# Kernel optimization log

Hardware: AMD Instinct MI355X
Metric: run time of the kernel (lower is better)

The kernel has to match this reference:

```python
import jax, jax.numpy as jnp
import numpy as np

B, N, VF, EF, DV, DE, LN = 64, 64, 32, 16, 128, 128, 4
EPS_INNER = 128.0  # BatchNorm1d(MAX_N, internal_d_vert): 2nd positional arg is eps (faithful to source bug)
EPS_BN = 1e-5


def gev_layer(v_in, e_in, evW, evb, eW, eb, vW, vb, relu=True):
    act = jax.nn.relu if relu else (lambda x: x)
    ev = v_in @ evW + evb                                   # [B,N,De]
    # outer_v_sum: ev.unsqueeze(1) + ev.unsqueeze(2) -> [B,N,N,De]
    e_out = act(e_in @ eW + eb + ev[:, None, :, :] + ev[:, :, None, :])
    per_v_e = e_out.sum(axis=1)                             # sum-aggregate over dim 1
    v_out = act(jnp.concatenate([per_v_e, v_in], axis=-1) @ vW + vb)
    return v_out, e_out


def bn_flat(v, g, b):
    # BatchNorm1d(N*VF) on [B, N*VF] in training mode (biased var)
    x = v.reshape(-1, N * VF)
    mu = x.mean(axis=0)
    var = x.var(axis=0)
    x = (x - mu) * jax.lax.rsqrt(var + EPS_BN) * g + b
    return x.reshape(-1, N, VF)


def bn_inner(v, g, b):
    # BatchNorm1d(MAX_N, eps=128) on [B, N, D]: channels are the N axis, stats over (B, D)
    mu = v.mean(axis=(0, 2), keepdims=True)
    var = v.var(axis=(0, 2), keepdims=True)
    return (v - mu) * jax.lax.rsqrt(var + EPS_INNER) * g[None, :, None] + b[None, :, None]


def setup_inputs() -> dict:
    key = jax.random.key(0)
    ks = jax.random.split(key, 24)
    s = 0.01  # force_lin_init with init_noise=0.01, biases zero
    nrm = lambda k, shp: jax.random.normal(k, shp, dtype=jnp.float32) * s
    inp = {
        "v": jax.random.normal(ks[0], (B, N, VF), dtype=jnp.float32),
        "e": jax.random.normal(ks[1], (B, N, N, EF), dtype=jnp.float32),
        "bn_in_g": jnp.ones((N * VF,), jnp.float32),
        "bn_in_b": jnp.zeros((N * VF,), jnp.float32),
        "g1_evW": nrm(ks[2], (VF, DE)), "g1_evb": jnp.zeros((DE,), jnp.float32),
        "g1_eW": nrm(ks[3], (EF, DE)), "g1_eb": jnp.zeros((DE,), jnp.float32),
        "g1_vW": nrm(ks[4], (VF + DE, DV)), "g1_vb": jnp.zeros((DV,), jnp.float32),
        "inn_evW": nrm(ks[5], (LN, DV, DE)), "inn_evb": jnp.zeros((LN, DE), jnp.float32),
        "inn_eW": nrm(ks[6], (LN, DE, DE)), "inn_eb": jnp.zeros((LN, DE), jnp.float32),
        "inn_vW": nrm(ks[7], (LN, DV + DE, DV)), "inn_vb": jnp.zeros((LN, DV), jnp.float32),
        "bn_g": jnp.ones((LN, N), jnp.float32),
        "bn_b": jnp.zeros((LN, N), jnp.float32),
        "g3_evW": nrm(ks[8], (DV, 1)), "g3_evb": jnp.zeros((1,), jnp.float32),
        "g3_eW": nrm(ks[9], (DE, 1)), "g3_eb": jnp.zeros((1,), jnp.float32),
        "g3_vW": nrm(ks[10], (DV + 1, 1)), "g3_vb": jnp.zeros((1,), jnp.float32),
    }
    return inp


def reference(v, e, bn_in_g, bn_in_b, g1_evW, g1_evb, g1_eW, g1_eb, g1_vW, g1_vb,
              inn_evW, inn_evb, inn_eW, inn_eb, inn_vW, inn_vb, bn_g, bn_b,
              g3_evW, g3_evb, g3_eW, g3_eb, g3_vW, g3_vb):
    v = bn_flat(v, bn_in_g, bn_in_b)
    v, e = gev_layer(v, e, g1_evW, g1_evb, g1_eW, g1_eb, g1_vW, g1_vb)
    for i in range(LN):
        v_next, e_next = gev_layer(v, e, inn_evW[i], inn_evb[i], inn_eW[i], inn_eb[i], inn_vW[i], inn_vb[i])
        v = v_next + v  # resnet
        e = e_next + e
        v = bn_inner(v, bn_g[i], bn_b[i])
    v, e = gev_layer(v, e, g3_evW, g3_evb, g3_eW, g3_eb, g3_vW, g3_vb, relu=False)
    return v, e
```

## Files before the change

### kernel.cpp

```cpp
#include <hip/hip_runtime.h>
#include <hip/hip_bf16.h>


typedef __bf16 bf16_t;
typedef __bf16 bf16x8 __attribute__((ext_vector_type(8)));
typedef __bf16 bf16x4 __attribute__((ext_vector_type(4)));
typedef float f32x4 __attribute__((ext_vector_type(4)));

__device__ __forceinline__ void bar_lgkm() {
  asm volatile("s_waitcnt lgkmcnt(0)\n\ts_barrier" ::: "memory");
}

__global__ __launch_bounds__(256) void k_prep(const float* __restrict__ vin,
    const float* __restrict__ g, const float* __restrict__ bt,
    const float* __restrict__ eW, float* __restrict__ v0,
    bf16_t* __restrict__ Wt, float* __restrict__ stats) {
  const int blk = blockIdx.x, tid = threadIdx.x;
  if (blk < 8) {
    int ch = blk * 256 + tid;
    float s = 0.f, s2 = 0.f;
    for (int b = 0; b < 64; ++b) { float x = vin[b * 2048 + ch]; s += x; s2 += x * x; }
    float mu = s * (1.f / 64.f);
    float var = s2 * (1.f / 64.f) - mu * mu;
    float sc = rsqrtf(var + 1e-5f) * g[ch];
    float bb = bt[ch];
    for (int b = 0; b < 64; ++b) {
      float x = vin[b * 2048 + ch];
      v0[b * 2048 + ch] = (x - mu) * sc + bb;
    }
  } else if (blk < 264) {
    int idx = (blk - 8) * 256 + tid;
    int l = idx >> 14, r = idx & 16383, n = r >> 7, k = r & 127;
    Wt[idx] = (bf16_t)eW[(l << 14) + (k << 7) + n];
  } else {
    for (int i = tid; i < 512; i += 256) stats[i] = 0.f;
  }
}

template <int K>
__global__ __launch_bounds__(256) void k_ev(const float* __restrict__ v_in,
    const float* __restrict__ W, const float* __restrict__ bias,
    float* __restrict__ out) {
  __shared__ float rows_s[8][K];
  const int r0 = blockIdx.x * 8;
  const int tid = threadIdx.x;
  const int c = tid & 127, h = tid >> 7;
  for (int idx = tid; idx < 8 * K; idx += 256) {
    int rr = idx / K, kk = idx % K;
    rows_s[rr][kk] = v_in[(r0 + rr) * K + kk];
  }
  __syncthreads();
  float acc[4];
  const float bv = bias[c];
#pragma unroll
  for (int r = 0; r < 4; ++r) acc[r] = bv;
  for (int k4 = 0; k4 < K; k4 += 4) {
    float w0 = W[(k4 + 0) * 128 + c], w1 = W[(k4 + 1) * 128 + c];
    float w2 = W[(k4 + 2) * 128 + c], w3 = W[(k4 + 3) * 128 + c];
#pragma unroll
    for (int r = 0; r < 4; ++r) {
      float4 x = *(const float4*)&rows_s[h * 4 + r][k4];
      acc[r] += x.x * w0 + x.y * w1 + x.z * w2 + x.w * w3;
    }
  }
#pragma unroll
  for (int r = 0; r < 4; ++r) out[(r0 + h * 4 + r) * 128 + c] = acc[r];
}

__global__ __launch_bounds__(256) void k_evbn(float* __restrict__ v,
    const float* __restrict__ stats, const float* __restrict__ g,
    const float* __restrict__ bt, const float* __restrict__ W,
    const float* __restrict__ bias, float* __restrict__ out) {
  __shared__ float rows_s[8][128];
  const int r0 = blockIdx.x * 8;
  const int tid = threadIdx.x;
  const int c = tid & 127, h = tid >> 7;
#pragma unroll
  for (int u = 0; u < 4; ++u) {
    int idx = u * 256 + tid;
    int rr = idx >> 7, k = idx & 127;
    int n = (r0 + rr) & 63;
    float mu = stats[n] * (1.f / 8192.f);
    float var = stats[64 + n] * (1.f / 8192.f) - mu * mu;
    float sc = rsqrtf(var + 128.f) * g[n];
    float x = (v[(r0 + rr) * 128 + k] - mu) * sc + bt[n];
    rows_s[rr][k] = x;
    v[(r0 + rr) * 128 + k] = x;
  }
  __syncthreads();
  float acc[4];
  const float bv = bias[c];
#pragma unroll
  for (int r = 0; r < 4; ++r) acc[r] = bv;
  for (int k4 = 0; k4 < 128; k4 += 4) {
    float w0 = W[(k4 + 0) * 128 + c], w1 = W[(k4 + 1) * 128 + c];
    float w2 = W[(k4 + 2) * 128 + c], w3 = W[(k4 + 3) * 128 + c];
#pragma unroll
    for (int r = 0; r < 4; ++r) {
      float4 x = *(const float4*)&rows_s[h * 4 + r][k4];
      acc[r] += x.x * w0 + x.y * w1 + x.z * w2 + x.w * w3;
    }
  }
#pragma unroll
  for (int r = 0; r < 4; ++r) out[(r0 + h * 4 + r) * 128 + c] = acc[r];
}

__global__ __launch_bounds__(256) void k_edge_g1(const float* __restrict__ e0,
    const float* __restrict__ eW, const float* __restrict__ eb,
    const float* __restrict__ ev, bf16_t* __restrict__ e_ws,
    float* __restrict__ pve) {
  __shared__ bf16_t A0s[2][64][40];
  __shared__ bf16_t Os[2][64][136];
  const int b = blockIdx.x >> 5, j0 = (blockIdx.x & 31) * 2;
  const int tid = threadIdx.x;
  const int lane = tid & 63, w = tid >> 6;
  const int quad = lane >> 4, l16 = lane & 15;
#pragma unroll
  for (int t = 0; t < 2; ++t) {
    int idx = tid + t * 256;
    int row = idx >> 3, off = (idx & 7) * 4;
    int jc = off >> 4, k = off & 15;
    f32x4 x = *(const f32x4*)&e0[((b * 64 + row) * 64 + j0) * 16 + off];
    bf16x4 y;
#pragma unroll
    for (int r = 0; r < 4; ++r) y[r] = (bf16_t)x[r];
    *(bf16x4*)&A0s[jc][row][k] = y;
    bf16x4 z = {(bf16_t)0.f, (bf16_t)0.f, (bf16_t)0.f, (bf16_t)0.f};
    *(bf16x4*)&A0s[jc][row][16 + k] = z;
  }
  const int c0[2] = {w * 32 + quad * 4, w * 32 + 16 + quad * 4};
  bf16x8 wf[2];
#pragma unroll
  for (int nt = 0; nt < 2; ++nt) {
    const int c = w * 32 + nt * 16 + l16;
#pragma unroll
    for (int jj = 0; jj < 8; ++jj)
      wf[nt][jj] = (quad < 2) ? (bf16_t)eW[(quad * 8 + jj) * 128 + c] : (bf16_t)0.f;
  }
  f32x4 acc[2][4][2];
  {
    f32x4 ebv[2], evj[2][2], evi[4][2];
#pragma unroll
    for (int nt = 0; nt < 2; ++nt) {
      ebv[nt] = *(const f32x4*)&eb[c0[nt]];
#pragma unroll
      for (int jc = 0; jc < 2; ++jc)
        evj[jc][nt] = *(const f32x4*)&ev[(b * 64 + j0 + jc) * 128 + c0[nt]];
#pragma unroll
      for (int mt = 0; mt < 4; ++mt)
        evi[mt][nt] = *(const f32x4*)&ev[(b * 64 + mt * 16 + l16) * 128 + c0[nt]];
    }
#pragma unroll
    for (int jc = 0; jc < 2; ++jc)
#pragma unroll
      for (int mt = 0; mt < 4; ++mt)
#pragma unroll
        for (int nt = 0; nt < 2; ++nt)
          acc[jc][mt][nt] = ebv[nt] + evj[jc][nt] + evi[mt][nt];
  }
  __syncthreads();
#pragma unroll
  for (int jc = 0; jc < 2; ++jc) {
#pragma unroll
    for (int mt = 0; mt < 4; ++mt) {
      bf16x8 ef = *(const bf16x8*)&A0s[jc][mt * 16 + l16][quad * 8];
#pragma unroll
      for (int nt = 0; nt < 2; ++nt)
        acc[jc][mt][nt] = __builtin_amdgcn_mfma_f32_16x16x32_bf16(wf[nt], ef, acc[jc][mt][nt], 0, 0, 0);
    }
  }
#pragma unroll
  for (int jc = 0; jc < 2; ++jc) {
#pragma unroll
    for (int nt = 0; nt < 2; ++nt) {
      f32x4 ps = {0.f, 0.f, 0.f, 0.f};
#pragma unroll
      for (int mt = 0; mt < 4; ++mt) {
        const int i = mt * 16 + l16;
        bf16x4 outv;
#pragma unroll
        for (int r = 0; r < 4; ++r) {
          float vv = fmaxf(acc[jc][mt][nt][r], 0.f);
          ps[r] += vv;
          outv[r] = (bf16_t)vv;
        }
        *(bf16x4*)&Os[jc][i][c0[nt]] = outv;
      }
#pragma unroll
      for (int m = 1; m <= 8; m <<= 1) {
#pragma unroll
        for (int r = 0; r < 4; ++r) ps[r] += __shfl_xor(ps[r], m);
      }
      if (l16 == 0) *(f32x4*)&pve[(b * 64 + j0 + jc) * 128 + c0[nt]] = ps;
    }
  }
  __syncthreads();
  {
    bf16_t* ebase = &e_ws[((size_t)(b * 64 + j0) * 64) * 128];
#pragma unroll
    for (int t = 0; t < 8; ++t) {
      int idx = tid + t * 256;
      *(int4*)&ebase[idx * 8] =
          *(const int4*)&Os[idx >> 10][(idx >> 4) & 63][(idx & 15) * 8];
    }
  }
}

__global__ __launch_bounds__(256) void k_vg1_ev(const float* __restrict__ pve,
    const float* __restrict__ v0, const float* __restrict__ vW,
    const float* __restrict__ vb, const float* __restrict__ evW,
    const float* __restrict__ evb, float* __restrict__ v, float* __restrict__ ev) {
  __shared__ float in_s[8][160];
  __shared__ float vr[8][128];
  const int r0 = blockIdx.x * 8;
  const int tid = threadIdx.x;
  const int c = tid & 127, h = tid >> 7;
#pragma unroll
  for (int u = 0; u < 4; ++u) {
    int idx = u * 256 + tid;
    int rr = idx >> 7, k = idx & 127;
    in_s[rr][k] = pve[(r0 + rr) * 128 + k];
  }
  {
    int rr = tid >> 5, k = tid & 31;
    in_s[rr][128 + k] = v0[(r0 + rr) * 32 + k];
  }
  __syncthreads();
  float acc[4];
  const float bv = vb[c];
#pragma unroll
  for (int r = 0; r < 4; ++r) acc[r] = bv;
  for (int k4 = 0; k4 < 160; k4 += 4) {
    float w0 = vW[(k4 + 0) * 128 + c], w1 = vW[(k4 + 1) * 128 + c];
    float w2 = vW[(k4 + 2) * 128 + c], w3 = vW[(k4 + 3) * 128 + c];
#pragma unroll
    for (int r = 0; r < 4; ++r) {
      float4 x = *(const float4*)&in_s[h * 4 + r][k4];
      acc[r] += x.x * w0 + x.y * w1 + x.z * w2 + x.w * w3;
    }
  }
#pragma unroll
  for (int r = 0; r < 4; ++r) {
    float val = fmaxf(acc[r], 0.f);
    vr[h * 4 + r][c] = val;
    v[(r0 + h * 4 + r) * 128 + c] = val;
  }
  __syncthreads();
  float acc2[4];
  const float bv2 = evb[c];
#pragma unroll
  for (int r = 0; r < 4; ++r) acc2[r] = bv2;
  for (int k4 = 0; k4 < 128; k4 += 4) {
    float w0 = evW[(k4 + 0) * 128 + c], w1 = evW[(k4 + 1) * 128 + c];
    float w2 = evW[(k4 + 2) * 128 + c], w3 = evW[(k4 + 3) * 128 + c];
#pragma unroll
    for (int r = 0; r < 4; ++r) {
      float4 x = *(const float4*)&vr[h * 4 + r][k4];
      acc2[r] += x.x * w0 + x.y * w1 + x.z * w2 + x.w * w3;
    }
  }
#pragma unroll
  for (int r = 0; r < 4; ++r) ev[(r0 + h * 4 + r) * 128 + c] = acc2[r];
}

template <bool LAST>
__global__ __launch_bounds__(256) void k_edge_inner(bf16_t* __restrict__ e_ws,
    const bf16_t* __restrict__ Wt, const float* __restrict__ eb,
    const float* __restrict__ ev, float* __restrict__ pve,
    const float* __restrict__ eW3, float* __restrict__ edt) {
  __shared__ bf16_t As[2][64][136];
  __shared__ float W3s[128];
  const int b = blockIdx.x >> 5, j0 = (blockIdx.x & 31) * 2;
  const int tid = threadIdx.x;
  const int lane = tid & 63, w = tid >> 6;
  const int quad = lane >> 4, l16 = lane & 15;
  bf16_t* ebase = &e_ws[((size_t)(b * 64 + j0) * 64) * 128];
  int4 stg[8];
#pragma unroll
  for (int t = 0; t < 8; ++t) {
    int idx = tid + t * 256;
    stg[t] = *(const int4*)&ebase[idx * 8];
  }
  if (LAST) {
    if (tid < 128) W3s[tid] = eW3[tid];
  }
  bf16x8 wf[2][4];
#pragma unroll
  for (int nt = 0; nt < 2; ++nt)
#pragma unroll
    for (int ks = 0; ks < 4; ++ks)
      wf[nt][ks] = *(const bf16x8*)&Wt[(w * 32 + nt * 16 + l16) * 128 + ks * 32 + quad * 8];
  const int c0[2] = {w * 32 + quad * 4, w * 32 + 16 + quad * 4};
  f32x4 acc[2][4][2];
  {
    f32x4 ebv[2], evj[2][2], evi[4][2];
#pragma unroll
    for (int nt = 0; nt < 2; ++nt) {
      ebv[nt] = *(const f32x4*)&eb[c0[nt]];
#pragma unroll
      for (int jc = 0; jc < 2; ++jc)
        evj[jc][nt] = *(const f32x4*)&ev[(b * 64 + j0 + jc) * 128 + c0[nt]];
#pragma unroll
      for (int mt = 0; mt < 4; ++mt)
        evi[mt][nt] = *(const f32x4*)&ev[(b * 64 + mt * 16 + l16) * 128 + c0[nt]];
    }
#pragma unroll
    for (int jc = 0; jc < 2; ++jc)
#pragma unroll
      for (int mt = 0; mt < 4; ++mt)
#pragma unroll
        for (int nt = 0; nt < 2; ++nt)
          acc[jc][mt][nt] = ebv[nt] + evj[jc][nt] + evi[mt][nt];
  }
#pragma unroll
  for (int t = 0; t < 8; ++t) {
    int idx = tid + t * 256;
    *(int4*)&As[idx >> 10][(idx >> 4) & 63][(idx & 15) * 8] = stg[t];
  }
  bar_lgkm();
#pragma unroll
  for (int ks = 0; ks < 4; ++ks) {
    bf16x8 ef[2][4];
#pragma unroll
    for (int jc = 0; jc < 2; ++jc)
#pragma unroll
      for (int mt = 0; mt < 4; ++mt)
        ef[jc][mt] = *(const bf16x8*)&As[jc][mt * 16 + l16][ks * 32 + quad * 8];
#pragma unroll
    for (int jc = 0; jc < 2; ++jc)
#pragma unroll
      for (int mt = 0; mt < 4; ++mt)
#pragma unroll
        for (int nt = 0; nt < 2; ++nt)
          acc[jc][mt][nt] = __builtin_amdgcn_mfma_f32_16x16x32_bf16(wf[nt][ks], ef[jc][mt], acc[jc][mt][nt], 0, 0, 0);
  }
  bar_lgkm();
#pragma unroll
  for (int jc = 0; jc < 2; ++jc) {
#pragma unroll
    for (int nt = 0; nt < 2; ++nt) {
      f32x4 ps = {0.f, 0.f, 0.f, 0.f};
#pragma unroll
      for (int mt = 0; mt < 4; ++mt) {
        const int i = mt * 16 + l16;
        bf16x4 eo = *(const bf16x4*)&As[jc][i][c0[nt]];
        bf16x4 outv;
#pragma unroll
        for (int r = 0; r < 4; ++r) {
          float vv = fmaxf(acc[jc][mt][nt][r], 0.f);
          ps[r] += vv;
          outv[r] = (bf16_t)(vv + (float)eo[r]);
        }
        *(bf16x4*)&As[jc][i][c0[nt]] = outv;
      }
#pragma unroll
      for (int m = 1; m <= 8; m <<= 1) {
#pragma unroll
        for (int r = 0; r < 4; ++r) ps[r] += __shfl_xor(ps[r], m);
      }
      if (l16 == 0) *(f32x4*)&pve[(b * 64 + j0 + jc) * 128 + c0[nt]] = ps;
    }
  }
  bar_lgkm();
  if (!LAST) {
#pragma unroll
    for (int t = 0; t < 8; ++t) {
      int idx = tid + t * 256;
      *(int4*)&ebase[idx * 8] =
          *(const int4*)&As[idx >> 10][(idx >> 4) & 63][(idx & 15) * 8];
    }
  } else {
    const int i = tid >> 2, q = tid & 3;
#pragma unroll
    for (int jc = 0; jc < 2; ++jc) {
      float d = 0.f;
#pragma unroll
      for (int t = 0; t < 4; ++t) {
        bf16x8 x = *(const bf16x8*)&As[jc][i][q * 32 + t * 8];
#pragma unroll
        for (int u = 0; u < 8; ++u) d += (float)x[u] * W3s[q * 32 + t * 8 + u];
      }
      d += __shfl_xor(d, 1);
      d += __shfl_xor(d, 2);
      if (q == 0) edt[(b * 64 + j0 + jc) * 64 + i] = d;
    }
  }
}

__global__ __launch_bounds__(256) void k_v_inner(const float* __restrict__ pve,
    float* __restrict__ v, const float* __restrict__ vW,
    const float* __restrict__ vb, float* __restrict__ stats) {
  __shared__ float in_s[8][256];
  __shared__ float outs[8][132];
  __shared__ float part[16][2];
  const int r0 = blockIdx.x * 8;
  const int tid = threadIdx.x;
  const int c = tid & 127, h = tid >> 7;
#pragma unroll
  for (int u = 0; u < 4; ++u) {
    int idx = u * 256 + tid;
    int rr = idx >> 7, k = idx & 127;
    in_s[rr][k] = pve[(r0 + rr) * 128 + k];
    in_s[rr][128 + k] = v[(r0 + rr) * 128 + k];
  }
  __syncthreads();
  float acc[4];
  const float bv = vb[c];
#pragma unroll
  for (int r = 0; r < 4; ++r) acc[r] = bv;
  for (int k4 = 0; k4 < 256; k4 += 4) {
    float w0 = vW[(k4 + 0) * 128 + c], w1 = vW[(k4 + 1) * 128 + c];
    float w2 = vW[(k4 + 2) * 128 + c], w3 = vW[(k4 + 3) * 128 + c];
#pragma unroll
    for (int r = 0; r < 4; ++r) {
      float4 x = *(const float4*)&in_s[h * 4 + r][k4];
      acc[r] += x.x * w0 + x.y * w1 + x.z * w2 + x.w * w3;
    }
  }
#pragma unroll
  for (int r = 0; r < 4; ++r) {
    float val = fmaxf(acc[r], 0.f) + in_s[h * 4 + r][128 + c];
    outs[h * 4 + r][c] = val;
    v[(r0 + h * 4 + r) * 128 + c] = val;
  }
  __syncthreads();
  if (tid < 16) {
    int rr = tid >> 1, half = tid & 1;
    float s = 0.f, s2 = 0.f;
    for (int k = 0; k < 64; ++k) {
      float x = outs[rr][half * 64 + k];
      s += x; s2 += x * x;
    }
    part[tid][0] = s;
    part[tid][1] = s2;
  }
  __syncthreads();
  if (tid < 8) {
    int n = (r0 + tid) & 63;
    atomicAdd(&stats[n], part[tid * 2][0] + part[tid * 2 + 1][0]);
    atomicAdd(&stats[64 + n], part[tid * 2][1] + part[tid * 2 + 1][1]);
  }
}

__global__ __launch_bounds__(256) void k_g3(const float* __restrict__ vv,
    const float* __restrict__ stats3, const float* __restrict__ g,
    const float* __restrict__ bt, const float* __restrict__ evW3,
    const float* __restrict__ evb3, const float* __restrict__ eb3,
    const float* __restrict__ edt, const float* __restrict__ vW3,
    const float* __restrict__ vb3, float* __restrict__ out_v,
    float* __restrict__ out_e) {
  __shared__ float vbn[64][132];
  __shared__ float edts[64][68];
  __shared__ float scs[64], shs[64];
  __shared__ float W3e[128];
  __shared__ float vWs[132];
  __shared__ float ev3s[64];
  __shared__ float pj[4][64];
  const int b = blockIdx.x, tid = threadIdx.x;
  if (tid < 64) {
    float mu = stats3[tid] * (1.f / 8192.f);
    float var = stats3[64 + tid] * (1.f / 8192.f) - mu * mu;
    float sc = rsqrtf(var + 128.f) * g[tid];
    scs[tid] = sc;
    shs[tid] = bt[tid] - mu * sc;
  }
  if (tid < 128) W3e[tid] = evW3[tid];
  if (tid < 129) vWs[tid] = vW3[tid];
  __syncthreads();
#pragma unroll
  for (int t = 0; t < 8; ++t) {
    int idx = t * 1024 + tid * 4;
    int row = idx >> 7, cc = idx & 127;
    f32x4 x = *(const f32x4*)&vv[(b * 64 + row) * 128 + cc];
    *(f32x4*)&vbn[row][cc] = x * scs[row] + shs[row];
  }
#pragma unroll
  for (int t = 0; t < 4; ++t) {
    int idx = t * 1024 + tid * 4;
    int j = idx >> 6, i = idx & 63;
    *(f32x4*)&edts[j][i] = *(const f32x4*)&edt[(b * 64 + j) * 64 + i];
  }
  __syncthreads();
  {
    int i = tid >> 2, q = tid & 3;
    float d = 0.f;
#pragma unroll
    for (int u = 0; u < 32; ++u) d += vbn[i][q * 32 + u] * W3e[q * 32 + u];
    d += __shfl_xor(d, 1);
    d += __shfl_xor(d, 2);
    if (q == 0) ev3s[i] = d + evb3[0];
  }
  __syncthreads();
  {
    int q = tid >> 6, j = tid & 63;
    float s = 0.f;
    const float e3 = eb3[0];
    const float evj = ev3s[j];
#pragma unroll
    for (int r = 0; r < 16; ++r) {
      int i = q * 16 + r;
      float val = edts[j][i] + e3 + ev3s[i] + evj;
      out_e[(b * 64 + i) * 64 + j] = val;
      s += val;
    }
    pj[q][j] = s;
  }
  __syncthreads();
  {
    int n = tid >> 2, q = tid & 3;
    float d = 0.f;
#pragma unroll
    for (int u = 0; u < 32; ++u) d += vbn[n][q * 32 + u] * vWs[1 + q * 32 + u];
    d += __shfl_xor(d, 1);
    d += __shfl_xor(d, 2);
    if (q == 0) {
      float p3 = pj[0][n] + pj[1][n] + pj[2][n] + pj[3][n];
      out_v[b * 64 + n] = d + p3 * vWs[0] + vb3[0];
    }
  }
}

extern "C" void kernel_launch(void* const* d_in, const int* in_sizes, int n_in,
                              void* d_out, int out_size, void* d_ws, size_t ws_size,
                              hipStream_t stream) {
  const float* in_v    = (const float*)d_in[0];
  const float* in_e    = (const float*)d_in[1];
  const float* bn_in_g = (const float*)d_in[2];
  const float* bn_in_b = (const float*)d_in[3];
  const float* g1_evW  = (const float*)d_in[4];
  const float* g1_evb  = (const float*)d_in[5];
  const float* g1_eW   = (const float*)d_in[6];
  const float* g1_eb   = (const float*)d_in[7];
  const float* g1_vW   = (const float*)d_in[8];
  const float* g1_vb   = (const float*)d_in[9];
  const float* inn_evW = (const float*)d_in[10];
  const float* inn_evb = (const float*)d_in[11];
  const float* inn_eW  = (const float*)d_in[12];
  const float* inn_eb  = (const float*)d_in[13];
  const float* inn_vW  = (const float*)d_in[14];
  const float* inn_vb  = (const float*)d_in[15];
  const float* bn_g    = (const float*)d_in[16];
  const float* bn_b    = (const float*)d_in[17];
  const float* g3_evW  = (const float*)d_in[18];
  const float* g3_evb  = (const float*)d_in[19];
  const float* g3_eW   = (const float*)d_in[20];
  const float* g3_eb   = (const float*)d_in[21];
  const float* g3_vW   = (const float*)d_in[22];
  const float* g3_vb   = (const float*)d_in[23];

  char* ws = (char*)d_ws;
  bf16_t* e_ws = (bf16_t*)(ws);
  float* v     = (float*)(ws + 67108864);
  float* ev    = (float*)(ws + 69206016);
  float* pve   = (float*)(ws + 71303168);
  float* v0    = (float*)(ws + 73400320);
  bf16_t* Wt   = (bf16_t*)(ws + 73924608);
  float* edt   = (float*)(ws + 74055680);
  float* stats = (float*)(ws + 75104256);

  float* out_v = (float*)d_out;
  float* out_e = (float*)d_out + 4096;

  k_prep<<<265, 256, 0, stream>>>(in_v, bn_in_g, bn_in_b, inn_eW, v0, Wt, stats);

  k_ev<32><<<512, 256, 0, stream>>>(v0, g1_evW, g1_evb, ev);
  k_edge_g1<<<2048, 256, 0, stream>>>(in_e, g1_eW, g1_eb, ev, e_ws, pve);
  k_vg1_ev<<<512, 256, 0, stream>>>(pve, v0, g1_vW, g1_vb, inn_evW, inn_evb, v, ev);

  for (int l = 0; l < 4; ++l) {
    if (l > 0)
      k_evbn<<<512, 256, 0, stream>>>(v, stats + (l - 1) * 128, bn_g + (l - 1) * 64,
                                      bn_b + (l - 1) * 64, inn_evW + l * 16384,
                                      inn_evb + l * 128, ev);
    if (l < 3)
      k_edge_inner<false><<<2048, 256, 0, stream>>>(e_ws, Wt + l * 16384,
          inn_eb + l * 128, ev, pve, g3_eW, edt);
    else
      k_edge_inner<true><<<2048, 256, 0, stream>>>(e_ws, Wt + l * 16384,
          inn_eb + l * 128, ev, pve, g3_eW, edt);
    k_v_inner<<<512, 256, 0, stream>>>(pve, v, inn_vW + l * 32768, inn_vb + l * 128,
                                       stats + l * 128);
  }

  k_g3<<<64, 256, 0, stream>>>(v, stats + 384, bn_g + 192, bn_b + 192,
                               g3_evW, g3_evb, g3_eb, edt, g3_vW, g3_vb,
                               out_v, out_e);
}
```

Baseline: 367.7 us.

## Fuse vertex update GEMVs into edge kernels and drop separate vertex kernels

```diff
diff --git a/kernel.cpp b/kernel.cpp
--- a/kernel.cpp
+++ b/kernel.cpp
@@ -107,14 +107,22 @@
 
 __global__ __launch_bounds__(256) void k_edge_g1(const float* __restrict__ e0,
     const float* __restrict__ eW, const float* __restrict__ eb,
-    const float* __restrict__ ev, bf16_t* __restrict__ e_ws,
-    float* __restrict__ pve) {
+    const float* __restrict__ evA, bf16_t* __restrict__ e_ws,
+    const float* __restrict__ v0, const float* __restrict__ vW,
+    const float* __restrict__ vb, const float* __restrict__ evW,
+    const float* __restrict__ evb, float* __restrict__ v,
+    float* __restrict__ evB) {
   __shared__ bf16_t A0s[2][64][40];
   __shared__ bf16_t Os[2][64][136];
+  __shared__ float in_s[2][160];
+  __shared__ float vr_s[2][128];
   const int b = blockIdx.x >> 5, j0 = (blockIdx.x & 31) * 2;
   const int tid = threadIdx.x;
   const int lane = tid & 63, w = tid >> 6;
   const int quad = lane >> 4, l16 = lane & 15;
+  f32x4 v0reg;
+  if (tid < 16)
+    v0reg = *(const f32x4*)&v0[(b * 64 + j0 + (tid >> 3)) * 32 + (tid & 7) * 4];
 #pragma unroll
   for (int t = 0; t < 2; ++t) {
     int idx = tid + t * 256;
@@ -145,10 +153,10 @@
       ebv[nt] = *(const f32x4*)&eb[c0[nt]];
 #pragma unroll
       for (int jc = 0; jc < 2; ++jc)
-        evj[jc][nt] = *(const f32x4*)&ev[(b * 64 + j0 + jc) * 128 + c0[nt]];
+        evj[jc][nt] = *(const f32x4*)&evA[(b * 64 + j0 + jc) * 128 + c0[nt]];
 #pragma unroll
       for (int mt = 0; mt < 4; ++mt)
-        evi[mt][nt] = *(const f32x4*)&ev[(b * 64 + mt * 16 + l16) * 128 + c0[nt]];
+        evi[mt][nt] = *(const f32x4*)&evA[(b * 64 + mt * 16 + l16) * 128 + c0[nt]];
     }
 #pragma unroll
     for (int jc = 0; jc < 2; ++jc)
@@ -191,9 +199,10 @@
 #pragma unroll
         for (int r = 0; r < 4; ++r) ps[r] += __shfl_xor(ps[r], m);
       }
-      if (l16 == 0) *(f32x4*)&pve[(b * 64 + j0 + jc) * 128 + c0[nt]] = ps;
-    }
-  }
+      if (l16 == 0) *(f32x4*)&in_s[jc][c0[nt]] = ps;
+    }
+  }
+  if (tid < 16) *(f32x4*)&in_s[tid >> 3][128 + (tid & 7) * 4] = v0reg;
   __syncthreads();
   {
     bf16_t* ebase = &e_ws[((size_t)(b * 64 + j0) * 64) * 128];
@@ -204,72 +213,39 @@
           *(const int4*)&Os[idx >> 10][(idx >> 4) & 63][(idx & 15) * 8];
     }
   }
-}
-
-__global__ __launch_bounds__(256) void k_vg1_ev(const float* __restrict__ pve,
-    const float* __restrict__ v0, const float* __restrict__ vW,
-    const float* __restrict__ vb, const float* __restrict__ evW,
-    const float* __restrict__ evb, float* __restrict__ v, float* __restrict__ ev) {
-  __shared__ float in_s[8][160];
-  __shared__ float vr[8][128];
-  const int r0 = blockIdx.x * 8;
-  const int tid = threadIdx.x;
   const int c = tid & 127, h = tid >> 7;
-#pragma unroll
-  for (int u = 0; u < 4; ++u) {
-    int idx = u * 256 + tid;
-    int rr = idx >> 7, k = idx & 127;
-    in_s[rr][k] = pve[(r0 + rr) * 128 + k];
-  }
-  {
-    int rr = tid >> 5, k = tid & 31;
-    in_s[rr][128 + k] = v0[(r0 + rr) * 32 + k];
-  }
-  __syncthreads();
-  float acc[4];
-  const float bv = vb[c];
-#pragma unroll
-  for (int r = 0; r < 4; ++r) acc[r] = bv;
+  float vacc = vb[c];
   for (int k4 = 0; k4 < 160; k4 += 4) {
     float w0 = vW[(k4 + 0) * 128 + c], w1 = vW[(k4 + 1) * 128 + c];
     float w2 = vW[(k4 + 2) * 128 + c], w3 = vW[(k4 + 3) * 128 + c];
-#pragma unroll
-    for (int r = 0; r < 4; ++r) {
-      float4 x = *(const float4*)&in_s[h * 4 + r][k4];
-      acc[r] += x.x * w0 + x.y * w1 + x.z * w2 + x.w * w3;
-    }
-  }
-#pragma unroll
-  for (int r = 0; r < 4; ++r) {
-    float val = fmaxf(acc[r], 0.f);
-    vr[h * 4 + r][c] = val;
-    v[(r0 + h * 4 + r) * 128 + c] = val;
-  }
-  __syncthreads();
-  float acc2[4];
-  const float bv2 = evb[c];
-#pragma unroll
-  for (int r = 0; r < 4; ++r) acc2[r] = bv2;
+    float4 x = *(const float4*)&in_s[h][k4];
+    vacc += x.x * w0 + x.y * w1 + x.z * w2 + x.w * w3;
+  }
+  float vr = fmaxf(vacc, 0.f);
+  v[(b * 64 + j0 + h) * 128 + c] = vr;
+  vr_s[h][c] = vr;
+  __syncthreads();
+  float acc2 = evb[c];
   for (int k4 = 0; k4 < 128; k4 += 4) {
     float w0 = evW[(k4 + 0) * 128 + c], w1 = evW[(k4 + 1) * 128 + c];
     float w2 = evW[(k4 + 2) * 128 + c], w3 = evW[(k4 + 3) * 128 + c];
-#pragma unroll
-    for (int r = 0; r < 4; ++r) {
-      float4 x = *(const float4*)&vr[h * 4 + r][k4];
-      acc2[r] += x.x * w0 + x.y * w1 + x.z * w2 + x.w * w3;
-    }
-  }
-#pragma unroll
-  for (int r = 0; r < 4; ++r) ev[(r0 + h * 4 + r) * 128 + c] = acc2[r];
+    float4 x = *(const float4*)&vr_s[h][k4];
+    acc2 += x.x * w0 + x.y * w1 + x.z * w2 + x.w * w3;
+  }
+  evB[(b * 64 + j0 + h) * 128 + c] = acc2;
 }
 
 template <bool LAST>
 __global__ __launch_bounds__(256) void k_edge_inner(bf16_t* __restrict__ e_ws,
     const bf16_t* __restrict__ Wt, const float* __restrict__ eb,
-    const float* __restrict__ ev, float* __restrict__ pve,
-    const float* __restrict__ eW3, float* __restrict__ edt) {
+    const float* __restrict__ ev, const float* __restrict__ eW3,
+    float* __restrict__ edt, float* __restrict__ v,
+    const float* __restrict__ vW, const float* __restrict__ vb,
+    float* __restrict__ stats) {
   __shared__ bf16_t As[2][64][136];
   __shared__ float W3s[128];
+  __shared__ float in_s[2][256];
+  __shared__ float part[4][2];
   const int b = blockIdx.x >> 5, j0 = (blockIdx.x & 31) * 2;
   const int tid = threadIdx.x;
   const int lane = tid & 63, w = tid >> 6;
@@ -281,6 +257,9 @@
     int idx = tid + t * 256;
     stg[t] = *(const int4*)&ebase[idx * 8];
   }
+  f32x4 vreg;
+  if (tid < 64)
+    vreg = *(const f32x4*)&v[(b * 64 + j0 + (tid >> 5)) * 128 + (tid & 31) * 4];
   if (LAST) {
     if (tid < 128) W3s[tid] = eW3[tid];
   }
@@ -358,9 +337,10 @@
 #pragma unroll
         for (int r = 0; r < 4; ++r) ps[r] += __shfl_xor(ps[r], m);
       }
-      if (l16 == 0) *(f32x4*)&pve[(b * 64 + j0 + jc) * 128 + c0[nt]] = ps;
-    }
-  }
+      if (l16 == 0) *(f32x4*)&in_s[jc][c0[nt]] = ps;
+    }
+  }
+  if (tid < 64) *(f32x4*)&in_s[tid >> 5][128 + (tid & 31) * 4] = vreg;
   bar_lgkm();
   if (!LAST) {
 #pragma unroll
@@ -385,58 +365,26 @@
       if (q == 0) edt[(b * 64 + j0 + jc) * 64 + i] = d;
     }
   }
-}
-
-__global__ __launch_bounds__(256) void k_v_inner(const float* __restrict__ pve,
-    float* __restrict__ v, const float* __restrict__ vW,
-    const float* __restrict__ vb, float* __restrict__ stats) {
-  __shared__ float in_s[8][256];
-  __shared__ float outs[8][132];
-  __shared__ float part[16][2];
-  const int r0 = blockIdx.x * 8;
-  const int tid = threadIdx.x;
   const int c = tid & 127, h = tid >> 7;
-#pragma unroll
-  for (int u = 0; u < 4; ++u) {
-    int idx = u * 256 + tid;
-    int rr = idx >> 7, k = idx & 127;
-    in_s[rr][k] = pve[(r0 + rr) * 128 + k];
-    in_s[rr][128 + k] = v[(r0 + rr) * 128 + k];
-  }
-  __syncthreads();
-  float acc[4];
-  const float bv = vb[c];
-#pragma unroll
-  for (int r = 0; r < 4; ++r) acc[r] = bv;
+  float vacc = vb[c];
   for (int k4 = 0; k4 < 256; k4 += 4) {
     float w0 = vW[(k4 + 0) * 128 + c], w1 = vW[(k4 + 1) * 128 + c];
     float w2 = vW[(k4 + 2) * 128 + c], w3 = vW[(k4 + 3) * 128 + c];
-#pragma unroll
-    for (int r = 0; r < 4; ++r) {
-      float4 x = *(const float4*)&in_s[h * 4 + r][k4];
-      acc[r] += x.x * w0 + x.y * w1 + x.z * w2 + x.w * w3;
-    }
-  }
-#pragma unroll
-  for (int r = 0; r < 4; ++r) {
-    float val = fmaxf(acc[r], 0.f) + in_s[h * 4 + r][128 + c];
-    outs[h * 4 + r][c] = val;
-    v[(r0 + h * 4 + r) * 128 + c] = val;
-  }
-  __syncthreads();
-  if (tid < 16) {
-    int rr = tid >> 1, half = tid & 1;
-    float s = 0.f, s2 = 0.f;
-    for (int k = 0; k < 64; ++k) {
-      float x = outs[rr][half * 64 + k];
-      s += x; s2 += x * x;
-    }
-    part[tid][0] = s;
-    part[tid][1] = s2;
-  }
-  __syncthreads();
-  if (tid < 8) {
-    int n = (r0 + tid) & 63;
+    float4 x = *(const float4*)&in_s[h][k4];
+    vacc += x.x * w0 + x.y * w1 + x.z * w2 + x.w * w3;
+  }
+  float vnew = fmaxf(vacc, 0.f) + in_s[h][128 + c];
+  v[(b * 64 + j0 + h) * 128 + c] = vnew;
+  float s = vnew, s2 = vnew * vnew;
+#pragma unroll
+  for (int m = 1; m <= 32; m <<= 1) {
+    s += __shfl_xor(s, m);
+    s2 += __shfl_xor(s2, m);
+  }
+  if (lane == 0) { part[w][0] = s; part[w][1] = s2; }
+  bar_lgkm();
+  if (tid < 2) {
+    int n = j0 + tid;
     atomicAdd(&stats[n], part[tid * 2][0] + part[tid * 2 + 1][0]);
     atomicAdd(&stats[64 + n], part[tid * 2][1] + part[tid * 2 + 1][1]);
   }
@@ -551,8 +499,8 @@
   char* ws = (char*)d_ws;
   bf16_t* e_ws = (bf16_t*)(ws);
   float* v     = (float*)(ws + 67108864);
-  float* ev    = (float*)(ws + 69206016);
-  float* pve   = (float*)(ws + 71303168);
+  float* evA   = (float*)(ws + 69206016);
+  float* evB   = (float*)(ws + 71303168);
   float* v0    = (float*)(ws + 73400320);
   bf16_t* Wt   = (bf16_t*)(ws + 73924608);
   float* edt   = (float*)(ws + 74055680);
@@ -563,23 +511,23 @@
 
   k_prep<<<265, 256, 0, stream>>>(in_v, bn_in_g, bn_in_b, inn_eW, v0, Wt, stats);
 
-  k_ev<32><<<512, 256, 0, stream>>>(v0, g1_evW, g1_evb, ev);
-  k_edge_g1<<<2048, 256, 0, stream>>>(in_e, g1_eW, g1_eb, ev, e_ws, pve);
-  k_vg1_ev<<<512, 256, 0, stream>>>(pve, v0, g1_vW, g1_vb, inn_evW, inn_evb, v, ev);
+  k_ev<32><<<512, 256, 0, stream>>>(v0, g1_evW, g1_evb, evA);
+  k_edge_g1<<<2048, 256, 0, stream>>>(in_e, g1_eW, g1_eb, evA, e_ws,
+                                      v0, g1_vW, g1_vb, inn_evW, inn_evb, v, evB);
 
   for (int l = 0; l < 4; ++l) {
     if (l > 0)
       k_evbn<<<512, 256, 0, stream>>>(v, stats + (l - 1) * 128, bn_g + (l - 1) * 64,
                                       bn_b + (l - 1) * 64, inn_evW + l * 16384,
-                                      inn_evb + l * 128, ev);
+                                      inn_evb + l * 128, evB);
     if (l < 3)
       k_edge_inner<false><<<2048, 256, 0, stream>>>(e_ws, Wt + l * 16384,
-          inn_eb + l * 128, ev, pve, g3_eW, edt);
+          inn_eb + l * 128, evB, g3_eW, edt, v,
+          inn_vW + l * 32768, inn_vb + l * 128, stats + l * 128);
     else
       k_edge_inner<true><<<2048, 256, 0, stream>>>(e_ws, Wt + l * 16384,
-          inn_eb + l * 128, ev, pve, g3_eW, edt);
-    k_v_inner<<<512, 256, 0, stream>>>(pve, v, inn_vW + l * 32768, inn_vb + l * 128,
-                                       stats + l * 128);
+          inn_eb + l * 128, evB, g3_eW, edt, v,
+          inn_vW + l * 32768, inn_vb + l * 128, stats + l * 128);
   }
 
   k_g3<<<64, 256, 0, stream>>>(v, stats + 384, bn_g + 192, bn_b + 192,
```

Measured after the change: 396.2 us. 7.8% more time.
